# Performance work log

Measured on AMD Instinct MI355X. Metric: run time of the kernel, lower is better.

## Reference

```python
import jax, jax.numpy as jnp
import numpy as np

# Sizes
N, E = 100000, 3200000
F_NODE, F_EDGE, LD, HID, L = 4, 4, 6, 16, 8
ALPHA = 1.0
EPS = 1e-6


def setup_inputs() -> dict:
    key = jax.random.key(0)
    ks = jax.random.split(key, 8)
    x = jax.random.normal(ks[0], (N, F_NODE), jnp.float32)
    fixed_mask = jax.random.uniform(ks[1], (N,)) < 0.1
    x = x.at[:, -1].set(jnp.where(fixed_mask, jnp.abs(x[:, -1]) + 1.0, 0.0))
    # positive edge attributes (pipe resistance etc.)
    edge_attr = jax.random.uniform(ks[2], (E, F_EDGE), jnp.float32) * 0.9 + 0.1
    edge_index = jax.random.randint(ks[3], (2, E), 0, N, dtype=jnp.int64)
    d_in = 2 * LD + 2 * F_NODE + F_EDGE  # 24: [x_src, x_dst, attr_src, attr_dst, edge_attr]
    s = 0.1
    W1 = jax.random.normal(ks[4], (L, d_in, HID), jnp.float32) * s
    b1 = jnp.zeros((L, HID), jnp.float32)
    W2 = jax.random.normal(ks[5], (L, HID, LD), jnp.float32) * s
    b2 = jnp.zeros((L, LD), jnp.float32)
    Wf = jax.random.normal(ks[6], (LD, 1), jnp.float32) * s
    bf = jnp.zeros((1,), jnp.float32)
    return {"x": x, "edge_attr": edge_attr, "edge_index": edge_index,
            "W1": W1, "b1": b1, "W2": W2, "b2": b2, "Wf": Wf, "bf": bf}


def reference(x, edge_attr, edge_index, W1, b1, W2, b2, Wf, bf):
    src, dst = edge_index[0], edge_index[1]
    # in-degree for mean aggregation
    deg = jax.ops.segment_sum(jnp.ones((E,), jnp.float32), dst, num_segments=N)
    deg = jnp.maximum(deg, 1.0)
    X = jnp.zeros((N, LD), jnp.float32)
    na_src, na_dst = x[src], x[dst]  # static node-attr gathers reused each layer
    for l in range(L):  # num_convs GNNSConv layers
        m_in = jnp.concatenate([X[src], X[dst], na_src, na_dst, edge_attr], axis=-1)  # [E,24]
        h = jax.nn.relu(m_in @ W1[l] + b1[l])         # per-edge MLP hidden [E,16]
        m = h @ W2[l] + b2[l]                          # per-edge message [E,6]
        agg = jax.ops.segment_sum(m, dst, num_segments=N) / deg[:, None]  # mean aggr
        X = (1.0 - ALPHA) * X + ALPHA * agg            # latent update (alpha_update_x)
        X = jax.nn.relu(X)
    P = jax.nn.relu(X @ Wf + bf)                       # [N,1]
    fixed = x[:, -1]
    P_ = jnp.where(fixed != 0, fixed, P.reshape(-1))   # keep known pressures
    # BalanceConv: gas-network flow from squared-pressure drop, k = edge resistance
    dp2 = P_[src] ** 2 - P_[dst] ** 2
    k = edge_attr[:, 0]
    flows = jnp.sign(dp2) * jnp.sqrt(jnp.abs(dp2) / k + EPS)  # [E]
    inj = x[:, 0]  # nodal injection/demand
    balance = (jax.ops.segment_sum(flows, dst, num_segments=N)
               - jax.ops.segment_sum(flows, src, num_segments=N) + inj)
    imbalance = jnp.sqrt(jnp.sum(balance ** 2))
    return P, flows, jnp.stack([imbalance])
```

## Files before the change

### kernel.cpp

```cpp
#include <hip/hip_runtime.h>
#include <math.h>

#define N_NODES 100000
#define N_EDGES 3200000
#define F_NODE 4
#define F_EDGE 4
#define LD 6
#define HID 16
#define NLAYER 8
#define EPSF 1e-6f

#define NPB 64
#define NBK 1563
#define NBIN 196
#define G1 1000
#define CH (N_EDGES / G1)
#define EPT ((CH + 255) / 256)
#define SPLIT 4
#define NSB (NBIN * SPLIT)

__device__ __forceinline__ unsigned f2bf(float a, float b) {
    unsigned ua = __float_as_uint(a);
    ua = (ua + 0x7fffu + ((ua >> 16) & 1u)) >> 16;
    unsigned ub = __float_as_uint(b);
    ub = (ub + 0x7fffu + ((ub >> 16) & 1u)) & 0xffff0000u;
    return ua | ub;
}
__device__ __forceinline__ float bflo(unsigned u) { return __uint_as_float(u << 16); }
__device__ __forceinline__ float bfhi(unsigned u) { return __uint_as_float(u & 0xffff0000u); }

__global__ __launch_bounds__(256) void hist_kernel(const int* __restrict__ ei,
                                                   int* __restrict__ ghd,
                                                   int* __restrict__ ghs) {
    __shared__ int hd[NBIN];
    __shared__ int hs[NBIN];
    int t = threadIdx.x, blk = blockIdx.x;
    for (int i = t; i < NBIN; i += 256) { hd[i] = 0; hs[i] = 0; }
    __syncthreads();
    int beg = blk * CH, end = beg + CH;
    for (int e = beg + t; e < end; e += 256) {
        atomicAdd(&hs[ei[e] >> 9], 1);
        atomicAdd(&hd[ei[N_EDGES + e] >> 9], 1);
    }
    __syncthreads();
    for (int i = t; i < NBIN; i += 256) {
        ghd[(size_t)i * G1 + blk] = hd[i];
        ghs[(size_t)i * G1 + blk] = hs[i];
    }
}

__global__ __launch_bounds__(256) void scanb_kernel(int* __restrict__ ghd, int* __restrict__ ghs,
                                                    int* __restrict__ totd, int* __restrict__ tots) {
    __shared__ int part[256];
    int b = blockIdx.x, t = threadIdx.x;
#pragma unroll
    for (int a = 0; a < 2; a++) {
        int* g = a ? ghs : ghd;
        int vals[4];
        int sum = 0;
#pragma unroll
        for (int k = 0; k < 4; k++) {
            int idx = t * 4 + k;
            vals[k] = (idx < G1) ? g[(size_t)b * G1 + idx] : 0;
            sum += vals[k];
        }
        part[t] = sum;
        __syncthreads();
        for (int off = 1; off < 256; off <<= 1) {
            int v = (t >= off) ? part[t - off] : 0;
            __syncthreads();
            part[t] += v;
            __syncthreads();
        }
        int excl = part[t] - sum;
#pragma unroll
        for (int k = 0; k < 4; k++) {
            int idx = t * 4 + k;
            if (idx < G1) g[(size_t)b * G1 + idx] = excl;
            excl += vals[k];
        }
        if (t == 0) (a ? tots : totd)[b] = part[255];
        __syncthreads();
    }
}

__global__ __launch_bounds__(256) void totscan_kernel(const int* __restrict__ totd,
                                                      const int* __restrict__ tots,
                                                      int* __restrict__ binbased,
                                                      int* __restrict__ binbases) {
    __shared__ int part[256];
    int t = threadIdx.x;
#pragma unroll
    for (int a = 0; a < 2; a++) {
        const int* tot = a ? tots : totd;
        int* base = a ? binbases : binbased;
        int v = (t < NBIN) ? tot[t] : 0;
        part[t] = v;
        __syncthreads();
        for (int off = 1; off < 256; off <<= 1) {
            int u = (t >= off) ? part[t - off] : 0;
            __syncthreads();
            part[t] += u;
            __syncthreads();
        }
        if (t < NBIN) base[t] = part[t] - v;
        if (t == 0) base[NBIN] = N_EDGES;
        __syncthreads();
    }
}

__global__ __launch_bounds__(256) void scatterA_kernel(const int* __restrict__ ei,
                                                       const float* __restrict__ ea,
                                                       const int* __restrict__ ghd,
                                                       const int* __restrict__ ghs,
                                                       const int* __restrict__ binbased,
                                                       const int* __restrict__ binbases,
                                                       unsigned* __restrict__ aw0,
                                                       unsigned* __restrict__ aw1,
                                                       unsigned* __restrict__ aw2,
                                                       unsigned* __restrict__ sbufA) {
    __shared__ int hcnt[NBIN];
    __shared__ int cdl[NBIN];
    __shared__ int gb[NBIN];
    __shared__ int part[256];
    __shared__ unsigned st0[CH];
    __shared__ unsigned st1[CH];
    __shared__ unsigned st2[CH];
    __shared__ unsigned stg[CH];
    int t = threadIdx.x, blk = blockIdx.x;
    int beg = blk * CH;
    int lidx[EPT];

    for (int i = t; i < NBIN; i += 256) hcnt[i] = 0;
    __syncthreads();
    {
        int k = 0;
        for (int i = t; i < CH; i += 256, k++)
            lidx[k] = atomicAdd(&hcnt[ei[N_EDGES + beg + i] >> 9], 1);
    }
    __syncthreads();
    {
        int own = (t < NBIN) ? hcnt[t] : 0;
        part[t] = own;
        __syncthreads();
        for (int off = 1; off < 256; off <<= 1) {
            int v = (t >= off) ? part[t - off] : 0;
            __syncthreads();
            part[t] += v;
            __syncthreads();
        }
        if (t < NBIN) {
            cdl[t] = part[t] - own;
            gb[t] = binbased[t] + ghd[(size_t)t * G1 + blk];
        }
    }
    __syncthreads();
    {
        int k = 0;
        for (int i = t; i < CH; i += 256, k++) {
            int e = beg + i;
            int s = ei[e];
            int d = ei[N_EDGES + e];
            float4 ev = reinterpret_cast<const float4*>(ea)[e];
            int bin = d >> 9;
            int pos = cdl[bin] + lidx[k];
            st0[pos] = (unsigned)s | ((unsigned)(d & 511) << 17);
            st1[pos] = f2bf(ev.x, ev.y);
            st2[pos] = f2bf(ev.z, ev.w);
            stg[pos] = (unsigned)(gb[bin] + lidx[k]);
        }
    }
    __syncthreads();
    for (int i = t; i < CH; i += 256) {
        unsigned g = stg[i];
        aw0[g] = st0[i];
        aw1[g] = st1[i];
        aw2[g] = st2[i];
    }
    __syncthreads();

    for (int i = t; i < NBIN; i += 256) hcnt[i] = 0;
    __syncthreads();
    {
        int k = 0;
        for (int i = t; i < CH; i += 256, k++)
            lidx[k] = atomicAdd(&hcnt[ei[beg + i] >> 9], 1);
    }
    __syncthreads();
    {
        int own = (t < NBIN) ? hcnt[t] : 0;
        part[t] = own;
        __syncthreads();
        for (int off = 1; off < 256; off <<= 1) {
            int v = (t >= off) ? part[t - off] : 0;
            __syncthreads();
            part[t] += v;
            __syncthreads();
        }
        if (t < NBIN) {
            cdl[t] = part[t] - own;
            gb[t] = binbases[t] + ghs[(size_t)t * G1 + blk];
        }
    }
    __syncthreads();
    {
        int k = 0;
        for (int i = t; i < CH; i += 256, k++) {
            int e = beg + i;
            int s = ei[e];
            int bin = s >> 9;
            int pos = cdl[bin] + lidx[k];
            st0[pos] = (unsigned)e | ((unsigned)(s & 511) << 22);
            stg[pos] = (unsigned)(gb[bin] + lidx[k]);
        }
    }
    __syncthreads();
    for (int i = t; i < CH; i += 256)
        sbufA[stg[i]] = st0[i];
}

__global__ __launch_bounds__(256) void sr_hist(const unsigned* __restrict__ aw0,
                                               const int* __restrict__ binbased,
                                               int* __restrict__ srh) {
    __shared__ int hist[512];
    int bs = blockIdx.x, t = threadIdx.x;
    int b = bs >> 2, h = bs & 3;
    hist[t] = 0; hist[t + 256] = 0;
    __syncthreads();
    int beg = binbased[b], end = binbased[b + 1];
    int len = end - beg;
    int p0 = beg + (int)((long long)len * h / SPLIT);
    int p1 = beg + (int)((long long)len * (h + 1) / SPLIT);
    for (int i = p0 + t; i < p1; i += 256)
        atomicAdd(&hist[(aw0[i] >> 17) & 511u], 1);
    __syncthreads();
    int* g = srh + (size_t)bs * 512;
    g[t] = hist[t];
    g[t + 256] = hist[t + 256];
}

__global__ __launch_bounds__(256) void sr_scat(const unsigned* __restrict__ aw0,
                                               const unsigned* __restrict__ aw1,
                                               const unsigned* __restrict__ aw2,
                                               const int* __restrict__ binbased,
                                               const int* __restrict__ srh,
                                               unsigned* __restrict__ bw0,
                                               unsigned* __restrict__ bw1,
                                               unsigned* __restrict__ bw2,
                                               float* __restrict__ degInv,
                                               int* __restrict__ based_bk) {
    __shared__ int cur[512];
    __shared__ int part[256];
    int bs = blockIdx.x, t = threadIdx.x;
    int b = bs >> 2, h = bs & 3;
    int beg = binbased[b], end = binbased[b + 1];
    int j0 = 2 * t, j1 = 2 * t + 1;
    int tot0 = 0, tot1 = 0;
    const int* gb = srh + (size_t)(b << 2) * 512;
#pragma unroll
    for (int hh = 0; hh < SPLIT; hh++) {
        tot0 += gb[hh * 512 + j0];
        tot1 += gb[hh * 512 + j1];
    }
    int tsum = tot0 + tot1;
    part[t] = tsum;
    __syncthreads();
    for (int off = 1; off < 256; off <<= 1) {
        int v = (t >= off) ? part[t - off] : 0;
        __syncthreads();
        part[t] += v;
        __syncthreads();
    }
    int excl = part[t] - tsum;
    cur[j0] = beg + excl;
    cur[j1] = beg + excl + tot0;
    if (h == 0) {
        int node0 = b << 9;
        if (node0 + j0 < N_NODES) degInv[node0 + j0] = 1.0f / fmaxf((float)tot0, 1.0f);
        if (node0 + j1 < N_NODES) degInv[node0 + j1] = 1.0f / fmaxf((float)tot1, 1.0f);
        if ((t & 31) == 0) {
            int k = t >> 5;
            int node = node0 + (k << 6);
            if (node < N_NODES) based_bk[(b << 3) + k] = beg + excl;
        }
        if (b == NBIN - 1 && t == 0) based_bk[NBK] = N_EDGES;
    }
    __syncthreads();
    int lo = h << 7, hi = lo + 128;
    for (int i = beg + t; i < end; i += 256) {
        unsigned r0 = aw0[i];
        int nib = (int)((r0 >> 17) & 511u);
        if (nib >= lo && nib < hi) {
            int p = atomicAdd(&cur[nib], 1);
            bw0[p] = (r0 & 0x1FFFFu) | ((unsigned)(nib & 63) << 17);
            bw1[p] = aw1[i];
            bw2[p] = aw2[i];
        }
    }
}

__global__ __launch_bounds__(256) void ss_hist(const unsigned* __restrict__ sbufA,
                                               const int* __restrict__ binbases,
                                               int* __restrict__ ssh) {
    __shared__ int hist[512];
    int bs = blockIdx.x, t = threadIdx.x;
    int b = bs >> 2, h = bs & 3;
    hist[t] = 0; hist[t + 256] = 0;
    __syncthreads();
    int beg = binbases[b], end = binbases[b + 1];
    int len = end - beg;
    int p0 = beg + (int)((long long)len * h / SPLIT);
    int p1 = beg + (int)((long long)len * (h + 1) / SPLIT);
    for (int i = p0 + t; i < p1; i += 256)
        atomicAdd(&hist[(sbufA[i] >> 22) & 511u], 1);
    __syncthreads();
    int* g = ssh + (size_t)bs * 512;
    g[t] = hist[t];
    g[t + 256] = hist[t + 256];
}

__global__ __launch_bounds__(256) void ss_scat(const unsigned* __restrict__ sbufA,
                                               const int* __restrict__ binbases,
                                               const int* __restrict__ ssh,
                                               unsigned* __restrict__ sbufB,
                                               int* __restrict__ bases_bk) {
    __shared__ int cur[512];
    __shared__ int part[256];
    int bs = blockIdx.x, t = threadIdx.x;
    int b = bs >> 2, h = bs & 3;
    int beg = binbases[b], end = binbases[b + 1];
    int j0 = 2 * t, j1 = 2 * t + 1;
    int tot0 = 0, tot1 = 0;
    const int* gb = ssh + (size_t)(b << 2) * 512;
#pragma unroll
    for (int hh = 0; hh < SPLIT; hh++) {
        tot0 += gb[hh * 512 + j0];
        tot1 += gb[hh * 512 + j1];
    }
    int tsum = tot0 + tot1;
    part[t] = tsum;
    __syncthreads();
    for (int off = 1; off < 256; off <<= 1) {
        int v = (t >= off) ? part[t - off] : 0;
        __syncthreads();
        part[t] += v;
        __syncthreads();
    }
    int excl = part[t] - tsum;
    cur[j0] = beg + excl;
    cur[j1] = beg + excl + tot0;
    if (h == 0) {
        if ((t & 31) == 0) {
            int k = t >> 5;
            int node = (b << 9) + (k << 6);
            if (node < N_NODES) bases_bk[(b << 3) + k] = beg + excl;
        }
        if (b == NBIN - 1 && t == 0) bases_bk[NBK] = N_EDGES;
    }
    __syncthreads();
    int lo = h << 7, hi = lo + 128;
    for (int i = beg + t; i < end; i += 256) {
        unsigned w = sbufA[i];
        int nib = (int)((w >> 22) & 511u);
        if (nib >= lo && nib < hi) {
            int p = atomicAdd(&cur[nib], 1);
            sbufB[p] = (w & 0x3FFFFFu) | ((unsigned)(nib & 63) << 22);
        }
    }
}

__global__ __launch_bounds__(256) void ab_init(const float* __restrict__ x,
                                               const float* __restrict__ W1,
                                               const float* __restrict__ b1,
                                               unsigned* __restrict__ A,
                                               unsigned* __restrict__ B) {
    __shared__ float sW[8 * HID];
    __shared__ float sb[HID];
    int t = threadIdx.x;
    for (int i = t; i < 8 * HID; i += 256) sW[i] = W1[12 * HID + i];
    if (t < HID) sb[t] = b1[t];
    __syncthreads();
    int i = blockIdx.x * 256 + t;
    if (i >= N_NODES) return;
    float4 xv = reinterpret_cast<const float4*>(x)[i];
    float xf[4] = {xv.x, xv.y, xv.z, xv.w};
    float a[HID], bb[HID];
#pragma unroll
    for (int j = 0; j < HID; j++) { a[j] = sb[j]; bb[j] = 0.0f; }
#pragma unroll
    for (int r = 0; r < 4; r++) {
        float v = xf[r];
#pragma unroll
        for (int j = 0; j < HID; j++) {
            a[j]  = fmaf(v, sW[r * HID + j], a[j]);
            bb[j] = fmaf(v, sW[(4 + r) * HID + j], bb[j]);
        }
    }
    uint4* Ao = reinterpret_cast<uint4*>(A + (size_t)i * 8);
    Ao[0] = make_uint4(f2bf(a[0], a[1]), f2bf(a[2], a[3]), f2bf(a[4], a[5]), f2bf(a[6], a[7]));
    Ao[1] = make_uint4(f2bf(a[8], a[9]), f2bf(a[10], a[11]), f2bf(a[12], a[13]), f2bf(a[14], a[15]));
    uint4* Bo = reinterpret_cast<uint4*>(B + (size_t)i * 8);
    Bo[0] = make_uint4(f2bf(bb[0], bb[1]), f2bf(bb[2], bb[3]), f2bf(bb[4], bb[5]), f2bf(bb[6], bb[7]));
    Bo[1] = make_uint4(f2bf(bb[8], bb[9]), f2bf(bb[10], bb[11]), f2bf(bb[12], bb[13]), f2bf(bb[14], bb[15]));
}

template <int LAST>
__global__ __launch_bounds__(512) void edge_layer(const unsigned* __restrict__ bw0,
                                                  const unsigned* __restrict__ bw1,
                                                  const unsigned* __restrict__ bw2,
                                                  const unsigned* __restrict__ Ain,
                                                  const unsigned* __restrict__ Bin,
                                                  const float* __restrict__ x,
                                                  const float* __restrict__ degInv,
                                                  const float* __restrict__ W1l,
                                                  const float* __restrict__ W2l,
                                                  const float* __restrict__ b2l,
                                                  const float* __restrict__ W1n,
                                                  const float* __restrict__ b1n,
                                                  const float* __restrict__ Wf,
                                                  const float* __restrict__ bfp,
                                                  const int* __restrict__ based_bk,
                                                  unsigned* __restrict__ Aout,
                                                  unsigned* __restrict__ Bout,
                                                  float* __restrict__ Pout,
                                                  float* __restrict__ Pbuf) {
    __shared__ float sWea[4 * HID];
    __shared__ float sW2[HID * LD];
    __shared__ float sb2[LD];
    __shared__ float sW1n[20 * HID];
    __shared__ float sb1n[HID];
    __shared__ float sWf[LD];
    __shared__ float sbf;
    __shared__ float accf[NPB * 8];
    __shared__ unsigned sB[NPB * 8];
    int t = threadIdx.x;
    int b = blockIdx.x;
    for (int i = t; i < 4 * HID; i += 512) sWea[i] = W1l[20 * HID + i];
    for (int i = t; i < HID * LD; i += 512) sW2[i] = W2l[i];
    if (t < LD) sb2[t] = b2l[t];
    if (!LAST) {
        for (int i = t; i < 20 * HID; i += 512) sW1n[i] = W1n[i];
        if (t < HID) sb1n[t] = b1n[t];
    } else {
        if (t < LD) sWf[t] = Wf[t];
        if (t == 0) sbf = bfp[0];
    }
    if (t < NPB * 8) accf[t] = 0.0f;
    {
        size_t base8 = (size_t)(b << 6) * 8;
        for (int i = t; i < NPB * 8; i += 512) {
            size_t gi = base8 + i;
            sB[i] = (gi < (size_t)N_NODES * 8) ? Bin[gi] : 0u;
        }
    }
    __syncthreads();

    int beg = based_bk[b], end = based_bk[b + 1];
    int lane = t & 63;

    for (int base = beg; base < end; base += 512) {
        int p = base + t;
        bool valid = p < end;
        int key = -1;
        float out[LD];
#pragma unroll
        for (int o = 0; o < LD; o++) out[o] = 0.0f;

        if (valid) {
            unsigned r0 = bw0[p];
            unsigned w1 = bw1[p];
            unsigned w2 = bw2[p];
            int s = (int)(r0 & 0x1FFFFu);
            key = (int)((r0 >> 17) & 63u);
            const uint4* Ap = reinterpret_cast<const uint4*>(Ain + (size_t)s * 8);
            uint4 ax = Ap[0], ay = Ap[1];
            const uint4* Bp = reinterpret_cast<const uint4*>(sB) + (key << 1);
            uint4 bx = Bp[0], by = Bp[1];
            float h[HID];
            h[0]  = bflo(ax.x) + bflo(bx.x);  h[1]  = bfhi(ax.x) + bfhi(bx.x);
            h[2]  = bflo(ax.y) + bflo(bx.y);  h[3]  = bfhi(ax.y) + bfhi(bx.y);
            h[4]  = bflo(ax.z) + bflo(bx.z);  h[5]  = bfhi(ax.z) + bfhi(bx.z);
            h[6]  = bflo(ax.w) + bflo(bx.w);  h[7]  = bfhi(ax.w) + bfhi(bx.w);
            h[8]  = bflo(ay.x) + bflo(by.x);  h[9]  = bfhi(ay.x) + bfhi(by.x);
            h[10] = bflo(ay.y) + bflo(by.y);  h[11] = bfhi(ay.y) + bfhi(by.y);
            h[12] = bflo(ay.z) + bflo(by.z);  h[13] = bfhi(ay.z) + bfhi(by.z);
            h[14] = bflo(ay.w) + bflo(by.w);  h[15] = bfhi(ay.w) + bfhi(by.w);
            float ef[4] = {bflo(w1), bfhi(w1), bflo(w2), bfhi(w2)};
#pragma unroll
            for (int rr = 0; rr < 4; rr++) {
                float v = ef[rr];
#pragma unroll
                for (int j = 0; j < HID; j++) h[j] = fmaf(v, sWea[rr * HID + j], h[j]);
            }
#pragma unroll
            for (int j = 0; j < HID; j++) h[j] = fmaxf(h[j], 0.0f);
#pragma unroll
            for (int o = 0; o < LD; o++) out[o] = sb2[o];
#pragma unroll
            for (int j = 0; j < HID; j++) {
                float hj = h[j];
#pragma unroll
                for (int o = 0; o < LD; o++) out[o] = fmaf(hj, sW2[j * LD + o], out[o]);
            }
        }

#pragma unroll
        for (int st = 1; st < 64; st <<= 1) {
            int kup = __shfl_up(key, st, 64);
            bool same = (lane >= st) && (kup == key);
#pragma unroll
            for (int o = 0; o < LD; o++) {
                float v = __shfl_up(out[o], st, 64);
                if (same) out[o] += v;
            }
        }
        int knx = __shfl_down(key, 1, 64);
        bool tail = (lane == 63) || (knx != key);
        if (valid && tail) {
#pragma unroll
            for (int o = 0; o < LD; o++) atomicAdd(&accf[(key << 3) + o], out[o]);
        }
    }
    __syncthreads();

    if (t < NPB) {
        int gid = (b << 6) + t;
        if (gid < N_NODES) {
            float inv = degInv[gid];
            float Xv[LD];
#pragma unroll
            for (int o = 0; o < LD; o++) Xv[o] = fmaxf(accf[(t << 3) + o] * inv, 0.0f);
            if (LAST) {
                float a2 = sbf;
#pragma unroll
                for (int o = 0; o < LD; o++) a2 = fmaf(Xv[o], sWf[o], a2);
                float P = fmaxf(a2, 0.0f);
                Pout[gid] = P;
                float fx = x[gid * F_NODE + 3];
                Pbuf[gid] = (fx != 0.0f) ? fx : P;
            } else {
                float4 xv = reinterpret_cast<const float4*>(x)[gid];
                float xf[4] = {xv.x, xv.y, xv.z, xv.w};
                float a[HID], bb[HID];
#pragma unroll
                for (int j = 0; j < HID; j++) { a[j] = sb1n[j]; bb[j] = 0.0f; }
#pragma unroll
                for (int rr = 0; rr < LD; rr++) {
                    float v = Xv[rr];
#pragma unroll
                    for (int j = 0; j < HID; j++) {
                        a[j]  = fmaf(v, sW1n[rr * HID + j], a[j]);
                        bb[j] = fmaf(v, sW1n[(LD + rr) * HID + j], bb[j]);
                    }
                }
#pragma unroll
                for (int rr = 0; rr < 4; rr++) {
                    float v = xf[rr];
#pragma unroll
                    for (int j = 0; j < HID; j++) {
                        a[j]  = fmaf(v, sW1n[(12 + rr) * HID + j], a[j]);
                        bb[j] = fmaf(v, sW1n[(16 + rr) * HID + j], bb[j]);
                    }
                }
                uint4* Ao = reinterpret_cast<uint4*>(Aout + (size_t)gid * 8);
                Ao[0] = make_uint4(f2bf(a[0], a[1]), f2bf(a[2], a[3]), f2bf(a[4], a[5]), f2bf(a[6], a[7]));
                Ao[1] = make_uint4(f2bf(a[8], a[9]), f2bf(a[10], a[11]), f2bf(a[12], a[13]), f2bf(a[14], a[15]));
                uint4* Bo = reinterpret_cast<uint4*>(Bout + (size_t)gid * 8);
                Bo[0] = make_uint4(f2bf(bb[0], bb[1]), f2bf(bb[2], bb[3]), f2bf(bb[4], bb[5]), f2bf(bb[6], bb[7]));
                Bo[1] = make_uint4(f2bf(bb[8], bb[9]), f2bf(bb[10], bb[11]), f2bf(bb[12], bb[13]), f2bf(bb[14], bb[15]));
            }
        }
    }
}

__global__ __launch_bounds__(256) void flows_noatomic(const int* __restrict__ ei,
                                                      const float* __restrict__ ea,
                                                      const float* __restrict__ Pbuf,
                                                      float* __restrict__ flows_out) {
    int e = blockIdx.x * 256 + threadIdx.x;
    if (e >= N_EDGES) return;
    int s = ei[e];
    int d = ei[N_EDGES + e];
    float ps = Pbuf[s], pd = Pbuf[d];
    float dp2 = ps * ps - pd * pd;
    float k = ea[(size_t)e * F_EDGE];
    float sg = (dp2 > 0.0f) ? 1.0f : ((dp2 < 0.0f) ? -1.0f : 0.0f);
    flows_out[e] = sg * sqrtf(fabsf(dp2) / k + EPSF);
}

__global__ __launch_bounds__(256) void balance_in(const unsigned* __restrict__ bw0,
                                                  const unsigned* __restrict__ bw1,
                                                  const float* __restrict__ Pbuf,
                                                  const float* __restrict__ x,
                                                  const int* __restrict__ based_bk,
                                                  float* __restrict__ bal) {
    __shared__ float acc[NPB];
    __shared__ float pdl[NPB];
    int t = threadIdx.x;
    int b = blockIdx.x;
    if (t < NPB) {
        acc[t] = 0.0f;
        int gid = (b << 6) + t;
        pdl[t] = (gid < N_NODES) ? Pbuf[gid] : 0.0f;
    }
    __syncthreads();
    int beg = based_bk[b], end = based_bk[b + 1];
    int lane = t & 63;
    for (int base = beg; base < end; base += 256) {
        int p = base + t;
        bool valid = p < end;
        int key = -1;
        float f = 0.0f;
        if (valid) {
            unsigned r0 = bw0[p];
            int s = (int)(r0 & 0x1FFFFu);
            key = (int)((r0 >> 17) & 63u);
            float ps = Pbuf[s];
            float pd = pdl[key];
            float k = bflo(bw1[p]);
            float dp2 = ps * ps - pd * pd;
            float sg = (dp2 > 0.0f) ? 1.0f : ((dp2 < 0.0f) ? -1.0f : 0.0f);
            f = sg * sqrtf(fabsf(dp2) / k + EPSF);
        }
#pragma unroll
        for (int st = 1; st < 64; st <<= 1) {
            int kup = __shfl_up(key, st, 64);
            float v = __shfl_up(f, st, 64);
            if ((lane >= st) && (kup == key)) f += v;
        }
        int knx = __shfl_down(key, 1, 64);
        bool tail = (lane == 63) || (knx != key);
        if (valid && tail) atomicAdd(&acc[key], f);
    }
    __syncthreads();
    if (t < NPB) {
        int gid = (b << 6) + t;
        if (gid < N_NODES) bal[gid] = acc[t] + x[gid * F_NODE + 0];
    }
}

__global__ __launch_bounds__(256) void balance_out(const unsigned* __restrict__ sbufB,
                                                   const float* __restrict__ flows,
                                                   const int* __restrict__ bases_bk,
                                                   const float* __restrict__ bal,
                                                   float* __restrict__ imb2) {
    __shared__ float acc[NPB];
    int t = threadIdx.x;
    if (t < NPB) acc[t] = 0.0f;
    __syncthreads();
    int b = blockIdx.x;
    int beg = bases_bk[b], end = bases_bk[b + 1];
    int lane = t & 63;
    for (int base = beg; base < end; base += 256) {
        int q = base + t;
        bool valid = q < end;
        int key = -1;
        float f = 0.0f;
        if (valid) {
            unsigned u = sbufB[q];
            key = (int)((u >> 22) & 63u);
            f = flows[u & 0x3FFFFFu];
        }
#pragma unroll
        for (int st = 1; st < 64; st <<= 1) {
            int kup = __shfl_up(key, st, 64);
            float v = __shfl_up(f, st, 64);
            if ((lane >= st) && (kup == key)) f += v;
        }
        int knx = __shfl_down(key, 1, 64);
        bool tail = (lane == 63) || (knx != key);
        if (valid && tail) atomicAdd(&acc[key], f);
    }
    __syncthreads();
    if (t < NPB) {
        float v = 0.0f;
        int gid = (b << 6) + t;
        if (gid < N_NODES) {
            float bv = bal[gid] - acc[t];
            v = bv * bv;
        }
#pragma unroll
        for (int off = 32; off > 0; off >>= 1) v += __shfl_down(v, off, 64);
        if (t == 0) atomicAdd(imb2, v);
    }
}

__global__ void fin_kernel(const float* __restrict__ imb2, float* __restrict__ out) {
    out[0] = sqrtf(imb2[0]);
}

extern "C" void kernel_launch(void* const* d_in, const int* in_sizes, int n_in,
                              void* d_out, int out_size, void* d_ws, size_t ws_size,
                              hipStream_t stream) {
    const float* x   = (const float*)d_in[0];
    const float* ea  = (const float*)d_in[1];
    const int*   ei  = (const int*)d_in[2];
    const float* W1  = (const float*)d_in[3];
    const float* b1  = (const float*)d_in[4];
    const float* W2  = (const float*)d_in[5];
    const float* b2  = (const float*)d_in[6];
    const float* Wf  = (const float*)d_in[7];
    const float* bf_ = (const float*)d_in[8];
    float* out = (float*)d_out;

    const size_t N = N_NODES, E = N_EDGES;

    size_t o = 0;
    auto alloc = [&](size_t n) { size_t r = o; o += (n + 3) & ~(size_t)3; return r; };
    size_t o_bw0      = alloc(E);
    size_t o_bw1      = alloc(E);
    size_t o_bw2      = alloc(E);
    size_t o_aw0      = alloc(E);
    size_t o_aw1      = alloc(E);
    size_t o_aw2      = alloc(E);
    size_t o_sbufA    = alloc(E);
    size_t o_ghd      = alloc((size_t)NBIN * G1);
    size_t o_ghs      = alloc((size_t)NBIN * G1);
    size_t o_srh      = alloc((size_t)NSB * 512);
    size_t o_ssh      = alloc((size_t)NSB * 512);
    size_t o_totd     = alloc(NBIN);
    size_t o_tots     = alloc(NBIN);
    size_t o_binbased = alloc(NBIN + 1);
    size_t o_binbases = alloc(NBIN + 1);
    size_t o_basedbk  = alloc(NBK + 1);
    size_t o_basesbk  = alloc(NBK + 1);
    size_t o_degInv   = alloc(N);
    size_t o_A0       = alloc(8 * N);
    size_t o_B0       = alloc(8 * N);
    size_t o_A1       = alloc(8 * N);
    size_t o_B1       = alloc(8 * N);
    size_t o_Pbuf     = alloc(N);
    size_t o_bal      = alloc(N);
    size_t o_imb2     = alloc(16);
    (void)o;

    int* wsi = (int*)d_ws;
    unsigned* bw0      = (unsigned*)(wsi + o_bw0);
    unsigned* bw1      = (unsigned*)(wsi + o_bw1);
    unsigned* bw2      = (unsigned*)(wsi + o_bw2);
    unsigned* aw0      = (unsigned*)(wsi + o_aw0);
    unsigned* aw1      = (unsigned*)(wsi + o_aw1);
    unsigned* aw2      = (unsigned*)(wsi + o_aw2);
    unsigned* sbufA    = (unsigned*)(wsi + o_sbufA);
    unsigned* sbufB    = (unsigned*)(wsi + o_aw0);
    int*      ghd      = wsi + o_ghd;
    int*      ghs      = wsi + o_ghs;
    int*      srh      = wsi + o_srh;
    int*      ssh      = wsi + o_ssh;
    int*      totd     = wsi + o_totd;
    int*      tots     = wsi + o_tots;
    int*      binbased = wsi + o_binbased;
    int*      binbases = wsi + o_binbases;
    int*      based_bk = wsi + o_basedbk;
    int*      bases_bk = wsi + o_basesbk;
    float*    degInv   = (float*)(wsi + o_degInv);
    unsigned* A0       = (unsigned*)(wsi + o_A0);
    unsigned* B0       = (unsigned*)(wsi + o_B0);
    unsigned* A1       = (unsigned*)(wsi + o_A1);
    unsigned* B1       = (unsigned*)(wsi + o_B1);
    float*    Pbuf     = (float*)(wsi + o_Pbuf);
    float*    bal      = (float*)(wsi + o_bal);
    float*    imb2     = (float*)(wsi + o_imb2);

    const int NB = (N_NODES + 255) / 256;
    const int EB = (N_EDGES + 255) / 256;

    hipMemsetAsync(imb2, 0, sizeof(float), stream);

    hist_kernel<<<G1, 256, 0, stream>>>(ei, ghd, ghs);
    scanb_kernel<<<NBIN, 256, 0, stream>>>(ghd, ghs, totd, tots);
    totscan_kernel<<<1, 256, 0, stream>>>(totd, tots, binbased, binbases);
    scatterA_kernel<<<G1, 256, 0, stream>>>(ei, ea, ghd, ghs, binbased, binbases,
                                            aw0, aw1, aw2, sbufA);
    sr_hist<<<NSB, 256, 0, stream>>>(aw0, binbased, srh);
    sr_scat<<<NSB, 256, 0, stream>>>(aw0, aw1, aw2, binbased, srh,
                                     bw0, bw1, bw2, degInv, based_bk);
    ss_hist<<<NSB, 256, 0, stream>>>(sbufA, binbases, ssh);
    ss_scat<<<NSB, 256, 0, stream>>>(sbufA, binbases, ssh, sbufB, bases_bk);

    ab_init<<<NB, 256, 0, stream>>>(x, W1, b1, A0, B0);

    for (int l = 0; l < NLAYER; l++) {
        const unsigned* Ain = (l & 1) ? A1 : A0;
        const unsigned* Bin = (l & 1) ? B1 : B0;
        unsigned* Aout = (l & 1) ? A0 : A1;
        unsigned* Bout = (l & 1) ? B0 : B1;
        const float* W1l = W1 + (size_t)l * 24 * HID;
        const float* W2l = W2 + (size_t)l * HID * LD;
        const float* b2l = b2 + (size_t)l * LD;
        if (l < NLAYER - 1) {
            edge_layer<0><<<NBK, 512, 0, stream>>>(bw0, bw1, bw2, Ain, Bin, x, degInv,
                                                   W1l, W2l, b2l,
                                                   W1 + (size_t)(l + 1) * 24 * HID,
                                                   b1 + (size_t)(l + 1) * HID,
                                                   Wf, bf_, based_bk,
                                                   Aout, Bout, out, Pbuf);
        } else {
            edge_layer<1><<<NBK, 512, 0, stream>>>(bw0, bw1, bw2, Ain, Bin, x, degInv,
                                                   W1l, W2l, b2l,
                                                   W1, b1, Wf, bf_, based_bk,
                                                   Aout, Bout, out, Pbuf);
        }
    }

    flows_noatomic<<<EB, 256, 0, stream>>>(ei, ea, Pbuf, out + N);
    balance_in<<<NBK, 256, 0, stream>>>(bw0, bw1, Pbuf, x, based_bk, bal);
    balance_out<<<NBK, 256, 0, stream>>>(sbufB, out + N, bases_bk, bal, imb2);
    fin_kernel<<<1, 1, 0, stream>>>(imb2, out + (size_t)N + E);
}
```

Before: 949.9 us.

## Stage radix scatter through LDS and process two edges per thread in layer kernel

The scatter kernels now place each sub-bin's entries in shared-memory staging buffers using local offsets, then write them out to global memory contiguously. Overflow beyond the staging capacity still goes straight to global memory. This is meant to replace scattered global writes with coalesced ones. The layer kernel now has each thread load two consecutive edges with 64-bit vector loads and accumulate them locally, flushing to shared memory when the destination key changes. That halves the thread iterations and segmented-scan passes, at the cost of more registers and a large LDS footprint that may lower occupancy in the scatter kernels.

```diff
diff --git a/kernel.cpp b/kernel.cpp
--- a/kernel.cpp
+++ b/kernel.cpp
@@ -18,6 +18,7 @@
 #define EPT ((CH + 255) / 256)
 #define SPLIT 4
 #define NSB (NBIN * SPLIT)
+#define SCAP 6144
 
 __device__ __forceinline__ unsigned f2bf(float a, float b) {
     unsigned ua = __float_as_uint(a);
@@ -249,18 +250,21 @@
                                                unsigned* __restrict__ bw2,
                                                float* __restrict__ degInv,
                                                int* __restrict__ based_bk) {
-    __shared__ int cur[512];
+    __shared__ int cur[128];
     __shared__ int part[256];
+    __shared__ int sSub[2];
+    __shared__ unsigned stw[SCAP];
+    __shared__ unsigned sti[SCAP];
     int bs = blockIdx.x, t = threadIdx.x;
     int b = bs >> 2, h = bs & 3;
     int beg = binbased[b], end = binbased[b + 1];
     int j0 = 2 * t, j1 = 2 * t + 1;
     int tot0 = 0, tot1 = 0;
-    const int* gb = srh + (size_t)(b << 2) * 512;
+    const int* gbh = srh + (size_t)(b << 2) * 512;
 #pragma unroll
     for (int hh = 0; hh < SPLIT; hh++) {
-        tot0 += gb[hh * 512 + j0];
-        tot1 += gb[hh * 512 + j1];
+        tot0 += gbh[hh * 512 + j0];
+        tot1 += gbh[hh * 512 + j1];
     }
     int tsum = tot0 + tot1;
     part[t] = tsum;
@@ -272,8 +276,12 @@
         __syncthreads();
     }
     int excl = part[t] - tsum;
-    cur[j0] = beg + excl;
-    cur[j1] = beg + excl + tot0;
+    int gcur0 = beg + excl;
+    int gcur1 = gcur0 + tot0;
+    int lo = h << 7, hi = lo + 128;
+    if (j0 == lo) sSub[0] = gcur0;
+    if (h < 3) { if (j0 == hi) sSub[1] = gcur0; }
+    else if (t == 0) sSub[1] = end;
     if (h == 0) {
         int node0 = b << 9;
         if (node0 + j0 < N_NODES) degInv[node0 + j0] = 1.0f / fmaxf((float)tot0, 1.0f);
@@ -286,16 +294,28 @@
         if (b == NBIN - 1 && t == 0) based_bk[NBK] = N_EDGES;
     }
     __syncthreads();
-    int lo = h << 7, hi = lo + 128;
+    int subbase = sSub[0];
+    if (j0 >= lo && j0 < hi) cur[j0 - lo] = gcur0 - subbase;
+    if (j1 >= lo && j1 < hi) cur[j1 - lo] = gcur1 - subbase;
+    __syncthreads();
     for (int i = beg + t; i < end; i += 256) {
         unsigned r0 = aw0[i];
         int nib = (int)((r0 >> 17) & 511u);
-        if (nib >= lo && nib < hi) {
-            int p = atomicAdd(&cur[nib], 1);
-            bw0[p] = (r0 & 0x1FFFFu) | ((unsigned)(nib & 63) << 17);
-            bw1[p] = aw1[i];
-            bw2[p] = aw2[i];
-        }
+        if ((nib >> 7) == h) {
+            int p = atomicAdd(&cur[nib & 127], 1);
+            unsigned w = (r0 & 0x1FFFFu) | ((unsigned)(nib & 63) << 17);
+            if (p < SCAP) { stw[p] = w; sti[p] = (unsigned)i; }
+            else { bw0[subbase + p] = w; bw1[subbase + p] = aw1[i]; bw2[subbase + p] = aw2[i]; }
+        }
+    }
+    __syncthreads();
+    int tot = sSub[1] - subbase;
+    if (tot > SCAP) tot = SCAP;
+    for (int i = t; i < tot; i += 256) {
+        unsigned idx = sti[i];
+        bw0[subbase + i] = stw[i];
+        bw1[subbase + i] = aw1[idx];
+        bw2[subbase + i] = aw2[idx];
     }
 }
 
@@ -324,18 +344,20 @@
                                                const int* __restrict__ ssh,
                                                unsigned* __restrict__ sbufB,
                                                int* __restrict__ bases_bk) {
-    __shared__ int cur[512];
+    __shared__ int cur[128];
     __shared__ int part[256];
+    __shared__ int sSub[2];
+    __shared__ unsigned stw[SCAP];
     int bs = blockIdx.x, t = threadIdx.x;
     int b = bs >> 2, h = bs & 3;
     int beg = binbases[b], end = binbases[b + 1];
     int j0 = 2 * t, j1 = 2 * t + 1;
     int tot0 = 0, tot1 = 0;
-    const int* gb = ssh + (size_t)(b << 2) * 512;
+    const int* gbh = ssh + (size_t)(b << 2) * 512;
 #pragma unroll
     for (int hh = 0; hh < SPLIT; hh++) {
-        tot0 += gb[hh * 512 + j0];
-        tot1 += gb[hh * 512 + j1];
+        tot0 += gbh[hh * 512 + j0];
+        tot1 += gbh[hh * 512 + j1];
     }
     int tsum = tot0 + tot1;
     part[t] = tsum;
@@ -347,8 +369,12 @@
         __syncthreads();
     }
     int excl = part[t] - tsum;
-    cur[j0] = beg + excl;
-    cur[j1] = beg + excl + tot0;
+    int gcur0 = beg + excl;
+    int gcur1 = gcur0 + tot0;
+    int lo = h << 7, hi = lo + 128;
+    if (j0 == lo) sSub[0] = gcur0;
+    if (h < 3) { if (j0 == hi) sSub[1] = gcur0; }
+    else if (t == 0) sSub[1] = end;
     if (h == 0) {
         if ((t & 31) == 0) {
             int k = t >> 5;
@@ -358,15 +384,25 @@
         if (b == NBIN - 1 && t == 0) bases_bk[NBK] = N_EDGES;
     }
     __syncthreads();
-    int lo = h << 7, hi = lo + 128;
+    int subbase = sSub[0];
+    if (j0 >= lo && j0 < hi) cur[j0 - lo] = gcur0 - subbase;
+    if (j1 >= lo && j1 < hi) cur[j1 - lo] = gcur1 - subbase;
+    __syncthreads();
     for (int i = beg + t; i < end; i += 256) {
         unsigned w = sbufA[i];
         int nib = (int)((w >> 22) & 511u);
-        if (nib >= lo && nib < hi) {
-            int p = atomicAdd(&cur[nib], 1);
-            sbufB[p] = (w & 0x3FFFFFu) | ((unsigned)(nib & 63) << 22);
-        }
-    }
+        if ((nib >> 7) == h) {
+            int p = atomicAdd(&cur[nib & 127], 1);
+            unsigned wc = (w & 0x3FFFFFu) | ((unsigned)(nib & 63) << 22);
+            if (p < SCAP) stw[p] = wc;
+            else sbufB[subbase + p] = wc;
+        }
+    }
+    __syncthreads();
+    int tot = sSub[1] - subbase;
+    if (tot > SCAP) tot = SCAP;
+    for (int i = t; i < tot; i += 256)
+        sbufB[subbase + i] = stw[i];
 }
 
 __global__ __launch_bounds__(256) void ab_init(const float* __restrict__ x,
@@ -456,51 +492,76 @@
     __syncthreads();
 
     int beg = based_bk[b], end = based_bk[b + 1];
+    int abeg = beg & ~1;
+    int nPairs = (end - abeg + 1) >> 1;
     int lane = t & 63;
 
-    for (int base = beg; base < end; base += 512) {
-        int p = base + t;
-        bool valid = p < end;
+    float out[LD];
+    auto edge_compute = [&](unsigned r0w, unsigned w1w, unsigned w2w, int key) {
+        int s = (int)(r0w & 0x1FFFFu);
+        const uint4* Ap = reinterpret_cast<const uint4*>(Ain + (size_t)s * 8);
+        uint4 ax = Ap[0], ay = Ap[1];
+        const uint4* Bp = reinterpret_cast<const uint4*>(sB) + (key << 1);
+        uint4 bx = Bp[0], by = Bp[1];
+        float h[HID];
+        h[0]  = bflo(ax.x) + bflo(bx.x);  h[1]  = bfhi(ax.x) + bfhi(bx.x);
+        h[2]  = bflo(ax.y) + bflo(bx.y);  h[3]  = bfhi(ax.y) + bfhi(bx.y);
+        h[4]  = bflo(ax.z) + bflo(bx.z);  h[5]  = bfhi(ax.z) + bfhi(bx.z);
+        h[6]  = bflo(ax.w) + bflo(bx.w);  h[7]  = bfhi(ax.w) + bfhi(bx.w);
+        h[8]  = bflo(ay.x) + bflo(by.x);  h[9]  = bfhi(ay.x) + bfhi(by.x);
+        h[10] = bflo(ay.y) + bflo(by.y);  h[11] = bfhi(ay.y) + bfhi(by.y);
+        h[12] = bflo(ay.z) + bflo(by.z);  h[13] = bfhi(ay.z) + bfhi(by.z);
+        h[14] = bflo(ay.w) + bflo(by.w);  h[15] = bfhi(ay.w) + bfhi(by.w);
+        float ef[4] = {bflo(w1w), bfhi(w1w), bflo(w2w), bfhi(w2w)};
+#pragma unroll
+        for (int rr = 0; rr < 4; rr++) {
+            float v = ef[rr];
+#pragma unroll
+            for (int j = 0; j < HID; j++) h[j] = fmaf(v, sWea[rr * HID + j], h[j]);
+        }
+#pragma unroll
+        for (int j = 0; j < HID; j++) h[j] = fmaxf(h[j], 0.0f);
+        float mo[LD];
+#pragma unroll
+        for (int o = 0; o < LD; o++) mo[o] = sb2[o];
+#pragma unroll
+        for (int j = 0; j < HID; j++) {
+            float hj = h[j];
+#pragma unroll
+            for (int o = 0; o < LD; o++) mo[o] = fmaf(hj, sW2[j * LD + o], mo[o]);
+        }
+#pragma unroll
+        for (int o = 0; o < LD; o++) out[o] += mo[o];
+    };
+
+    for (int pb = 0; pb < nPairs; pb += 512) {
+        int c = pb + t;
         int key = -1;
-        float out[LD];
 #pragma unroll
         for (int o = 0; o < LD; o++) out[o] = 0.0f;
 
-        if (valid) {
-            unsigned r0 = bw0[p];
-            unsigned w1 = bw1[p];
-            unsigned w2 = bw2[p];
-            int s = (int)(r0 & 0x1FFFFu);
-            key = (int)((r0 >> 17) & 63u);
-            const uint4* Ap = reinterpret_cast<const uint4*>(Ain + (size_t)s * 8);
-            uint4 ax = Ap[0], ay = Ap[1];
-            const uint4* Bp = reinterpret_cast<const uint4*>(sB) + (key << 1);
-            uint4 bx = Bp[0], by = Bp[1];
-            float h[HID];
-            h[0]  = bflo(ax.x) + bflo(bx.x);  h[1]  = bfhi(ax.x) + bfhi(bx.x);
-            h[2]  = bflo(ax.y) + bflo(bx.y);  h[3]  = bfhi(ax.y) + bfhi(bx.y);
-            h[4]  = bflo(ax.z) + bflo(bx.z);  h[5]  = bfhi(ax.z) + bfhi(bx.z);
-            h[6]  = bflo(ax.w) + bflo(bx.w);  h[7]  = bfhi(ax.w) + bfhi(bx.w);
-            h[8]  = bflo(ay.x) + bflo(by.x);  h[9]  = bfhi(ay.x) + bfhi(by.x);
-            h[10] = bflo(ay.y) + bflo(by.y);  h[11] = bfhi(ay.y) + bfhi(by.y);
-            h[12] = bflo(ay.z) + bflo(by.z);  h[13] = bfhi(ay.z) + bfhi(by.z);
-            h[14] = bflo(ay.w) + bflo(by.w);  h[15] = bfhi(ay.w) + bfhi(by.w);
-            float ef[4] = {bflo(w1), bfhi(w1), bflo(w2), bfhi(w2)};
-#pragma unroll
-            for (int rr = 0; rr < 4; rr++) {
-                float v = ef[rr];
-#pragma unroll
-                for (int j = 0; j < HID; j++) h[j] = fmaf(v, sWea[rr * HID + j], h[j]);
+        if (c < nPairs) {
+            int p0 = abeg + (c << 1);
+            uint2 r0 = *reinterpret_cast<const uint2*>(bw0 + p0);
+            uint2 w1 = *reinterpret_cast<const uint2*>(bw1 + p0);
+            uint2 w2 = *reinterpret_cast<const uint2*>(bw2 + p0);
+            if (p0 >= beg && p0 < end) {
+                key = (int)((r0.x >> 17) & 63u);
+                edge_compute(r0.x, w1.x, w2.x, key);
             }
-#pragma unroll
-            for (int j = 0; j < HID; j++) h[j] = fmaxf(h[j], 0.0f);
-#pragma unroll
-            for (int o = 0; o < LD; o++) out[o] = sb2[o];
-#pragma unroll
-            for (int j = 0; j < HID; j++) {
-                float hj = h[j];
-#pragma unroll
-                for (int o = 0; o < LD; o++) out[o] = fmaf(hj, sW2[j * LD + o], out[o]);
+            int p1 = p0 + 1;
+            if (p1 < end) {
+                int k1 = (int)((r0.y >> 17) & 63u);
+                if (k1 != key) {
+                    if (key >= 0) {
+#pragma unroll
+                        for (int o = 0; o < LD; o++) atomicAdd(&accf[(key << 3) + o], out[o]);
+#pragma unroll
+                        for (int o = 0; o < LD; o++) out[o] = 0.0f;
+                    }
+                    key = k1;
+                }
+                edge_compute(r0.y, w1.y, w2.y, key);
             }
         }
 
@@ -516,7 +577,7 @@
         }
         int knx = __shfl_down(key, 1, 64);
         bool tail = (lane == 63) || (knx != key);
-        if (valid && tail) {
+        if (tail && key >= 0) {
 #pragma unroll
             for (int o = 0; o < LD; o++) atomicAdd(&accf[(key << 3) + o], out[o]);
         }
```

Result: faster. 898.2 us (-5.4%).
